# Optimization experiments

Hardware: AMD Instinct MI355X
Metric: run time of the kernel (lower is better)

Reference implementation:

```python
import jax, jax.numpy as jnp
import numpy as np

D_MODEL = 1024
NUM_HEADS = 16
HEAD_DIM = D_MODEL // NUM_HEADS


def setup_inputs() -> dict:
    key = jax.random.key(0)
    kx, kq, kk, kv, ko = jax.random.split(key, 5)
    B, S = 4, 2048
    scale = 1.0 / np.sqrt(D_MODEL)
    return {
        "x": jax.random.normal(kx, (B, S, D_MODEL), dtype=jnp.float32),
        # bias-free linear weights, torch convention [out, in]
        "wq": jax.random.normal(kq, (D_MODEL, D_MODEL), dtype=jnp.float32) * scale,
        "wk": jax.random.normal(kk, (D_MODEL, D_MODEL), dtype=jnp.float32) * scale,
        "wv": jax.random.normal(kv, (D_MODEL, D_MODEL), dtype=jnp.float32) * scale,
        "wo": jax.random.normal(ko, (D_MODEL, D_MODEL), dtype=jnp.float32) * scale,
    }


def reference(x, wq, wk, wv, wo):
    B, S, D = x.shape
    H, Hd = NUM_HEADS, HEAD_DIM
    # projections (y = x @ W^T), reshape to [B, H, S, Hd]
    def proj(w):
        return jnp.einsum('bsd,ed->bse', x, w).reshape(B, S, H, Hd).transpose(0, 2, 1, 3)
    q, k, v = proj(wq), proj(wk), proj(wv)
    # scaled dot-product attention with causal mask
    scores = jnp.einsum('bhqd,bhkd->bhqk', q, k) / jnp.sqrt(jnp.asarray(Hd, x.dtype))
    causal = jnp.tril(jnp.ones((S, S), dtype=bool))  # [S, S]
    scores = jnp.where(causal[None, None], scores, jnp.asarray(-jnp.inf, x.dtype))
    attn = jax.nn.softmax(scores, axis=-1)
    out = jnp.einsum('bhqk,bhkd->bhqd', attn, v)  # [B, H, S, Hd]
    out = out.transpose(0, 2, 1, 3).reshape(B, S, D)
    return jnp.einsum('bsd,ed->bse', out, wo)
```

## Files before the change

### kernel.cpp

```cpp
#include <hip/hip_runtime.h>
#include <hip/hip_bf16.h>
#include <math.h>


#define S_LEN 2048
#define DM    1024
#define NH    16
#define HD    64
#define M_ROWS 8192

typedef __attribute__((ext_vector_type(8))) short bf16x8;
typedef __attribute__((ext_vector_type(4))) float f32x4;

__device__ __forceinline__ float bf2f(unsigned short u) {
  union { unsigned int i; float f; } c; c.i = ((unsigned int)u) << 16; return c.f;
}
__device__ __forceinline__ unsigned short f2bf(float f) {
  unsigned int x = __float_as_uint(f);
  if ((x & 0x7fffffffu) > 0x7f800000u) return (unsigned short)0x7fc0u;
  return (unsigned short)((x + 0x7fffu + ((x >> 16) & 1u)) >> 16);
}
__device__ __forceinline__ unsigned short f2bf_trunc(float f) {
  return (unsigned short)(__float_as_uint(f) >> 16);
}
__device__ __forceinline__ void gl_lds16(const unsigned short* g, unsigned short* l) {
  __builtin_amdgcn_global_load_lds(
      (const __attribute__((address_space(1))) unsigned int*)g,
      (__attribute__((address_space(3))) unsigned int*)l, 16, 0, 0);
}

#define FENCE() asm volatile("" ::: "memory")

__global__ __launch_bounds__(256) void cvt_bf16(const float* __restrict__ in,
                                                unsigned short* __restrict__ out) {
  const int i = blockIdx.x * 256 + threadIdx.x;
  float4 a = ((const float4*)in)[2 * i];
  float4 b = ((const float4*)in)[2 * i + 1];
  ushort4 r0, r1;
  r0.x = f2bf(a.x); r0.y = f2bf(a.y); r0.z = f2bf(a.z); r0.w = f2bf(a.w);
  r1.x = f2bf(b.x); r1.y = f2bf(b.y); r1.z = f2bf(b.z); r1.w = f2bf(b.w);
  ((ushort4*)out)[2 * i] = r0;
  ((ushort4*)out)[2 * i + 1] = r1;
}

__global__ __launch_bounds__(256) void cvt_w3(const float* __restrict__ w0,
                                              const float* __restrict__ w1,
                                              const float* __restrict__ w2,
                                              unsigned short* __restrict__ out) {
  const int idx = blockIdx.x;
  const int which = idx >> 9;
  const float* src = (which == 0) ? w0 : (which == 1) ? w1 : w2;
  unsigned short* dst = out + (size_t)which * (DM * DM);
  const int i = (idx & 511) * 256 + threadIdx.x;
  float4 a = ((const float4*)src)[2 * i];
  float4 b = ((const float4*)src)[2 * i + 1];
  ushort4 r0, r1;
  r0.x = f2bf(a.x); r0.y = f2bf(a.y); r0.z = f2bf(a.z); r0.w = f2bf(a.w);
  r1.x = f2bf(b.x); r1.y = f2bf(b.y); r1.z = f2bf(b.z); r1.w = f2bf(b.w);
  ((ushort4*)dst)[2 * i] = r0;
  ((ushort4*)dst)[2 * i + 1] = r1;
}

template <int OUT_MODE>
__global__ __launch_bounds__(512, 4) void gemm_bt(const unsigned short* __restrict__ A,
                                                  const unsigned short* __restrict__ Wall,
                                                  unsigned short* __restrict__ outB,
                                                  float* __restrict__ outF) {
  __shared__ __align__(16) unsigned short As[3 * 8192];
  __shared__ __align__(16) unsigned short Bs[3 * 4096];
  const int m0 = blockIdx.x * 256;
  const int n0 = blockIdx.y * 128;
  const int tid = threadIdx.x;
  const int lane = tid & 63, w = tid >> 6;
  const int quad = lane >> 4, l15 = lane & 15;
  const int wrow = w >> 1, wcol = w & 1;

  const int skg = w & 3, srq = w >> 2;
  const unsigned short* agA = A    + (size_t)(m0 + srq * 64 + lane) * DM + skg * 8;
  const unsigned short* bgB = Wall + (size_t)(n0 + srq * 64 + lane) * DM + skg * 8;
  const int lA0 = skg * 2048 + srq * 512;
  const int lA1 = lA0 + 1024;
  const int lB  = skg * 1024 + srq * 512;
  const int raA = quad * 2048 + (wrow * 64 + l15) * 8;
  const int raB = quad * 1024 + (wcol * 64 + l15) * 8;

  f32x4 acc[4][4];
#pragma unroll
  for (int i = 0; i < 4; ++i)
#pragma unroll
    for (int j = 0; j < 4; ++j) { acc[i][j].x = 0.f; acc[i][j].y = 0.f; acc[i][j].z = 0.f; acc[i][j].w = 0.f; }

#define STAGE3(T, SB) do {                                                   \
    const unsigned short* ap_ = agA + (size_t)(T) * 32;                      \
    gl_lds16(ap_,          &As[(SB) * 8192 + lA0]);                          \
    gl_lds16(ap_ + 131072, &As[(SB) * 8192 + lA1]);                          \
    gl_lds16(bgB + (size_t)(T) * 32, &Bs[(SB) * 4096 + lB]);                 \
  } while (0)

#define COMPUTE(CB) do {                                                     \
    bf16x8 af_[4], bq_[4];                                                   \
    _Pragma("unroll")                                                        \
    for (int mi = 0; mi < 4; ++mi)                                           \
      af_[mi] = *(const bf16x8*)&As[(CB) * 8192 + raA + mi * 128];           \
    _Pragma("unroll")                                                        \
    for (int ni = 0; ni < 4; ++ni)                                           \
      bq_[ni] = *(const bf16x8*)&Bs[(CB) * 4096 + raB + ni * 128];           \
    __builtin_amdgcn_s_setprio(1);                                           \
    _Pragma("unroll")                                                        \
    for (int mi = 0; mi < 4; ++mi)                                           \
      _Pragma("unroll")                                                      \
      for (int ni = 0; ni < 4; ++ni)                                         \
        acc[mi][ni] = __builtin_amdgcn_mfma_f32_16x16x32_bf16(af_[mi], bq_[ni], acc[mi][ni], 0, 0, 0); \
    __builtin_amdgcn_s_setprio(0);                                           \
  } while (0)

#define SUBSTEP(T, SB, CB) do {                                              \
    FENCE();                                                                 \
    STAGE3((T), (SB));                                                       \
    asm volatile("s_waitcnt vmcnt(6)" ::: "memory");                         \
    __builtin_amdgcn_s_barrier();                                            \
    FENCE();                                                                 \
    COMPUTE(CB);                                                             \
    FENCE();                                                                 \
    __builtin_amdgcn_s_barrier();                                            \
  } while (0)

  STAGE3(0, 0);
  STAGE3(1, 1);

  for (int t = 0; t < 30; t += 3) {
    SUBSTEP(t + 2, 2, 0);
    SUBSTEP(t + 3, 0, 1);
    SUBSTEP(t + 4, 1, 2);
  }
  asm volatile("s_waitcnt vmcnt(3)" ::: "memory");
  __builtin_amdgcn_s_barrier();
  FENCE();
  COMPUTE(0);
  FENCE();
  __builtin_amdgcn_s_barrier();
  asm volatile("s_waitcnt vmcnt(0)" ::: "memory");
  __builtin_amdgcn_s_barrier();
  FENCE();
  COMPUTE(1);

#undef SUBSTEP
#undef COMPUTE
#undef STAGE3

  const float oscale = (OUT_MODE == 0 && n0 < 1024) ? 0.125f : 1.0f;
#pragma unroll
  for (int mi = 0; mi < 4; ++mi) {
#pragma unroll
    for (int reg = 0; reg < 4; ++reg) {
      const int m = m0 + wrow * 64 + mi * 16 + quad * 4 + reg;
#pragma unroll
      for (int ni = 0; ni < 4; ++ni) {
        const int e = n0 + wcol * 64 + ni * 16 + l15;
        const float v = acc[mi][ni][reg];
        if (OUT_MODE == 0) {
          const int z = e >> 10;
          const int e10 = e & 1023;
          const int b = m >> 11, s = m & (S_LEN - 1);
          const int h = e10 >> 6, hd = e10 & 63;
          outB[(size_t)z * (M_ROWS * DM) +
               (((size_t)(b * NH + h)) * S_LEN + s) * HD + hd] = f2bf(v * oscale);
        } else {
          outF[(size_t)m * DM + e] = v;
        }
      }
    }
  }
}

__global__ __launch_bounds__(256) void attn_mfma(const unsigned short* __restrict__ Q,
                                                 const unsigned short* __restrict__ K,
                                                 const unsigned short* __restrict__ V,
                                                 unsigned short* __restrict__ O) {
  __shared__ unsigned short Ks[64][72];
  __shared__ unsigned short Vt[64][72];
  __shared__ unsigned short Pl[4][16][72];
  const int bh  = blockIdx.x;
  const int t   = blockIdx.y;
  const int tid = threadIdx.x;
  const int w    = tid >> 6;
  const int lane = tid & 63;
  const int quad = lane >> 4;
  const int l15  = lane & 15;

  const size_t base = (size_t)bh * S_LEN * HD;
  const int kr0 = tid >> 3, kc0 = (tid & 7) * 8;
  const int vs = (tid & 31) * 2, vh = (tid >> 5) * 8;
  const int b = bh >> 4, h = bh & 15;

  for (int phase = 0; phase < 2; ++phase) {
    const int bx  = phase ? (31 - t) : t;
    const int wq0 = bx * 64 + w * 16;

    bf16x8 qa[2];
#pragma unroll
    for (int st = 0; st < 2; ++st)
      qa[st] = *(const bf16x8*)(Q + base + (size_t)(wq0 + l15) * HD + st * 32 + quad * 8);

    f32x4 o[4];
#pragma unroll
    for (int sub = 0; sub < 4; ++sub) { o[sub].x = 0.f; o[sub].y = 0.f; o[sub].z = 0.f; o[sub].w = 0.f; }
    float l_i[4] = {0.f, 0.f, 0.f, 0.f};

    const int jtmax = bx;
    for (int jt = 0; jt <= jtmax; ++jt) {
      __syncthreads();
      {
        const unsigned short* kb = K + base + (size_t)jt * 64 * HD;
        const unsigned short* vb = V + base + (size_t)jt * 64 * HD;
        *(uint4*)&Ks[kr0][kc0]      = *(const uint4*)(kb + kr0 * HD + kc0);
        *(uint4*)&Ks[kr0 + 32][kc0] = *(const uint4*)(kb + (kr0 + 32) * HD + kc0);
        union { uint4 v; unsigned short u[8]; } r0, r1;
        r0.v = *(const uint4*)(vb + (size_t)vs * HD + vh);
        r1.v = *(const uint4*)(vb + (size_t)(vs + 1) * HD + vh);
#pragma unroll
        for (int j = 0; j < 8; ++j)
          *(unsigned int*)&Vt[vh + j][vs] = (unsigned int)r0.u[j] | ((unsigned int)r1.u[j] << 16);
      }
      __syncthreads();

      const int rel = jt * 64 - wq0;
      const bool partial = (rel >= -63);
      const int submax = partial ? (((15 - rel) >> 4) + 1) : 4;
      const int steps  = partial ? ((submax + 1) >> 1) : 2;

      f32x4 s[4];
#pragma unroll
      for (int sub = 0; sub < 4; ++sub) {
        if (sub < submax) {
          bf16x8 kb0 = *(const bf16x8*)&Ks[sub * 16 + l15][quad * 8];
          bf16x8 kb1 = *(const bf16x8*)&Ks[sub * 16 + l15][quad * 8 + 32];
          f32x4 acc = {0.f, 0.f, 0.f, 0.f};
          acc = __builtin_amdgcn_mfma_f32_16x16x32_bf16(qa[0], kb0, acc, 0, 0, 0);
          acc = __builtin_amdgcn_mfma_f32_16x16x32_bf16(qa[1], kb1, acc, 0, 0, 0);
          s[sub] = acc;
        }
      }

#pragma unroll
      for (int reg = 0; reg < 4; ++reg) {
        float ls = 0.f;
#pragma unroll
        for (int sub = 0; sub < 4; ++sub) {
          if (sub < submax) {
            float v = s[sub][reg];
            if (partial) {
              const int c = jt * 64 + sub * 16 + l15;
              const int r = wq0 + quad * 4 + reg;
              v = (r >= c) ? v : -1.0e30f;
            }
            const float p = __expf(v);
            ls += p;
            Pl[w][quad * 4 + reg][sub * 16 + l15] = f2bf_trunc(p);
          } else {
            Pl[w][quad * 4 + reg][sub * 16 + l15] = 0;
          }
        }
        l_i[reg] += ls;
      }

#pragma unroll
      for (int st = 0; st < 2; ++st) {
        if (st < steps) {
          bf16x8 pa = *(const bf16x8*)&Pl[w][l15][st * 32 + quad * 8];
#pragma unroll
          for (int sub = 0; sub < 4; ++sub) {
            bf16x8 vv = *(const bf16x8*)&Vt[sub * 16 + l15][st * 32 + quad * 8];
            o[sub] = __builtin_amdgcn_mfma_f32_16x16x32_bf16(pa, vv, o[sub], 0, 0, 0);
          }
        }
      }
    }

#pragma unroll
    for (int reg = 0; reg < 4; ++reg) {
      float lt = l_i[reg];
      lt += __shfl_xor(lt, 1);
      lt += __shfl_xor(lt, 2);
      lt += __shfl_xor(lt, 4);
      lt += __shfl_xor(lt, 8);
      const float inv = 1.0f / lt;
      const int sg = wq0 + quad * 4 + reg;
#pragma unroll
      for (int sub = 0; sub < 4; ++sub) {
        O[((size_t)(b * S_LEN + sg)) * DM + h * HD + sub * 16 + l15] = f2bf(o[sub][reg] * inv);
      }
    }
  }
}

extern "C" void kernel_launch(void* const* d_in, const int* in_sizes, int n_in,
                              void* d_out, int out_size, void* d_ws, size_t ws_size,
                              hipStream_t stream) {
  const float* x  = (const float*)d_in[0];
  const float* wq = (const float*)d_in[1];
  const float* wk = (const float*)d_in[2];
  const float* wv = (const float*)d_in[3];
  const float* wo = (const float*)d_in[4];

  unsigned short* Qb = (unsigned short*)d_ws;
  unsigned short* Kb = Qb + (size_t)M_ROWS * DM;
  unsigned short* Vb = Kb + (size_t)M_ROWS * DM;
  unsigned short* Xb = Vb + (size_t)M_ROWS * DM;
  unsigned short* Ob = Xb;
  (void)Kb; (void)Vb;

  unsigned short* Wstash = (unsigned short*)d_out;

  dim3 bb(256);
  dim3 gb(512);

  hipLaunchKernelGGL(cvt_bf16, dim3((M_ROWS * DM) / 2048), bb, 0, stream, x, Xb);
  hipLaunchKernelGGL(cvt_w3, dim3(3 * (DM * DM) / 2048), bb, 0, stream, wq, wk, wv, Wstash);
  hipLaunchKernelGGL((gemm_bt<0>), dim3(M_ROWS / 256, 3 * DM / 128), gb, 0, stream,
                     Xb, Wstash, Qb, (float*)nullptr);
  hipLaunchKernelGGL(attn_mfma, dim3(64, 16), bb, 0, stream, Qb, Qb + (size_t)M_ROWS * DM,
                     Qb + 2 * (size_t)M_ROWS * DM, Ob);
  hipLaunchKernelGGL(cvt_bf16, dim3((DM * DM) / 2048), bb, 0, stream, wo, Qb);
  hipLaunchKernelGGL((gemm_bt<1>), dim3(M_ROWS / 256, DM / 128), gb, 0, stream,
                     Ob, Qb, (unsigned short*)nullptr, (float*)d_out);
}
```

Before: 230.0 us.

## Prefetch next K/V tile into registers and transpose score MFMA for packed P stores

Loads the next K/V tile into registers while the current tile is computed, hiding global load latency behind the MFMA work. Swaps the MFMA operands so each lane holds four consecutive key scores for one query row, which lets P be written to LDS as packed uint2 stores and reduces the row-sum to a single accumulator with fewer shuffles. Uses v_perm to build the V transpose and bf16 packing, and raises wave priority around the MFMA sections. The cost is extra live registers for the prefetch and more complex lane bookkeeping for normalization.

```diff
diff --git a/kernel.cpp b/kernel.cpp
--- a/kernel.cpp
+++ b/kernel.cpp
@@ -19,9 +19,6 @@
   unsigned int x = __float_as_uint(f);
   if ((x & 0x7fffffffu) > 0x7f800000u) return (unsigned short)0x7fc0u;
   return (unsigned short)((x + 0x7fffu + ((x >> 16) & 1u)) >> 16);
-}
-__device__ __forceinline__ unsigned short f2bf_trunc(float f) {
-  return (unsigned short)(__float_as_uint(f) >> 16);
 }
 __device__ __forceinline__ void gl_lds16(const unsigned short* g, unsigned short* l) {
   __builtin_amdgcn_global_load_lds(
@@ -196,6 +193,7 @@
   for (int phase = 0; phase < 2; ++phase) {
     const int bx  = phase ? (31 - t) : t;
     const int wq0 = bx * 64 + w * 16;
+    const int qrow = wq0 + l15;
 
     bf16x8 qa[2];
 #pragma unroll
@@ -205,24 +203,43 @@
     f32x4 o[4];
 #pragma unroll
     for (int sub = 0; sub < 4; ++sub) { o[sub].x = 0.f; o[sub].y = 0.f; o[sub].z = 0.f; o[sub].w = 0.f; }
-    float l_i[4] = {0.f, 0.f, 0.f, 0.f};
+    float l_acc = 0.f;
 
     const int jtmax = bx;
+
+    uint4 krA, krB, vrA, vrB;
+    {
+      const unsigned short* kbp = K + base;
+      const unsigned short* vbp = V + base;
+      krA = *(const uint4*)(kbp + kr0 * HD + kc0);
+      krB = *(const uint4*)(kbp + (kr0 + 32) * HD + kc0);
+      vrA = *(const uint4*)(vbp + (size_t)vs * HD + vh);
+      vrB = *(const uint4*)(vbp + (size_t)(vs + 1) * HD + vh);
+    }
+
     for (int jt = 0; jt <= jtmax; ++jt) {
       __syncthreads();
+      *(uint4*)&Ks[kr0][kc0]      = krA;
+      *(uint4*)&Ks[kr0 + 32][kc0] = krB;
       {
-        const unsigned short* kb = K + base + (size_t)jt * 64 * HD;
-        const unsigned short* vb = V + base + (size_t)jt * 64 * HD;
-        *(uint4*)&Ks[kr0][kc0]      = *(const uint4*)(kb + kr0 * HD + kc0);
-        *(uint4*)&Ks[kr0 + 32][kc0] = *(const uint4*)(kb + (kr0 + 32) * HD + kc0);
-        union { uint4 v; unsigned short u[8]; } r0, r1;
-        r0.v = *(const uint4*)(vb + (size_t)vs * HD + vh);
-        r1.v = *(const uint4*)(vb + (size_t)(vs + 1) * HD + vh);
-#pragma unroll
-        for (int j = 0; j < 8; ++j)
-          *(unsigned int*)&Vt[vh + j][vs] = (unsigned int)r0.u[j] | ((unsigned int)r1.u[j] << 16);
+        const unsigned int* a0 = (const unsigned int*)&vrA;
+        const unsigned int* a1 = (const unsigned int*)&vrB;
+#pragma unroll
+        for (int i = 0; i < 4; ++i) {
+          *(unsigned int*)&Vt[vh + 2 * i][vs]     = __builtin_amdgcn_perm(a1[i], a0[i], 0x05040100u);
+          *(unsigned int*)&Vt[vh + 2 * i + 1][vs] = __builtin_amdgcn_perm(a1[i], a0[i], 0x07060302u);
+        }
       }
       __syncthreads();
+
+      if (jt < jtmax) {
+        const unsigned short* kbp = K + base + (size_t)(jt + 1) * 64 * HD;
+        const unsigned short* vbp = V + base + (size_t)(jt + 1) * 64 * HD;
+        krA = *(const uint4*)(kbp + kr0 * HD + kc0);
+        krB = *(const uint4*)(kbp + (kr0 + 32) * HD + kc0);
+        vrA = *(const uint4*)(vbp + (size_t)vs * HD + vh);
+        vrB = *(const uint4*)(vbp + (size_t)(vs + 1) * HD + vh);
+      }
 
       const int rel = jt * 64 - wq0;
       const bool partial = (rel >= -63);
@@ -230,40 +247,47 @@
       const int steps  = partial ? ((submax + 1) >> 1) : 2;
 
       f32x4 s[4];
+      __builtin_amdgcn_s_setprio(1);
 #pragma unroll
       for (int sub = 0; sub < 4; ++sub) {
         if (sub < submax) {
           bf16x8 kb0 = *(const bf16x8*)&Ks[sub * 16 + l15][quad * 8];
           bf16x8 kb1 = *(const bf16x8*)&Ks[sub * 16 + l15][quad * 8 + 32];
           f32x4 acc = {0.f, 0.f, 0.f, 0.f};
-          acc = __builtin_amdgcn_mfma_f32_16x16x32_bf16(qa[0], kb0, acc, 0, 0, 0);
-          acc = __builtin_amdgcn_mfma_f32_16x16x32_bf16(qa[1], kb1, acc, 0, 0, 0);
+          acc = __builtin_amdgcn_mfma_f32_16x16x32_bf16(kb0, qa[0], acc, 0, 0, 0);
+          acc = __builtin_amdgcn_mfma_f32_16x16x32_bf16(kb1, qa[1], acc, 0, 0, 0);
           s[sub] = acc;
         }
       }
-
-#pragma unroll
-      for (int reg = 0; reg < 4; ++reg) {
-        float ls = 0.f;
-#pragma unroll
-        for (int sub = 0; sub < 4; ++sub) {
-          if (sub < submax) {
-            float v = s[sub][reg];
+      __builtin_amdgcn_s_setprio(0);
+
+#pragma unroll
+      for (int sub = 0; sub < 4; ++sub) {
+        if (sub < submax) {
+          float p0, p1, p2, p3;
+          {
+            float v0 = s[sub][0], v1 = s[sub][1], v2 = s[sub][2], v3 = s[sub][3];
             if (partial) {
-              const int c = jt * 64 + sub * 16 + l15;
-              const int r = wq0 + quad * 4 + reg;
-              v = (r >= c) ? v : -1.0e30f;
+              const int kb = jt * 64 + sub * 16 + quad * 4;
+              v0 = (qrow >= kb)     ? v0 : -1.0e30f;
+              v1 = (qrow >= kb + 1) ? v1 : -1.0e30f;
+              v2 = (qrow >= kb + 2) ? v2 : -1.0e30f;
+              v3 = (qrow >= kb + 3) ? v3 : -1.0e30f;
             }
-            const float p = __expf(v);
-            ls += p;
-            Pl[w][quad * 4 + reg][sub * 16 + l15] = f2bf_trunc(p);
-          } else {
-            Pl[w][quad * 4 + reg][sub * 16 + l15] = 0;
+            p0 = __expf(v0); p1 = __expf(v1); p2 = __expf(v2); p3 = __expf(v3);
           }
-        }
-        l_i[reg] += ls;
-      }
-
+          l_acc += (p0 + p1) + (p2 + p3);
+          uint2 dd;
+          dd.x = __builtin_amdgcn_perm(__float_as_uint(p1), __float_as_uint(p0), 0x07060302u);
+          dd.y = __builtin_amdgcn_perm(__float_as_uint(p3), __float_as_uint(p2), 0x07060302u);
+          *(uint2*)&Pl[w][l15][sub * 16 + quad * 4] = dd;
+        } else {
+          uint2 zz; zz.x = 0u; zz.y = 0u;
+          *(uint2*)&Pl[w][l15][sub * 16 + quad * 4] = zz;
+        }
+      }
+
+      __builtin_amdgcn_s_setprio(1);
 #pragma unroll
       for (int st = 0; st < 2; ++st) {
         if (st < steps) {
@@ -275,20 +299,20 @@
           }
         }
       }
+      __builtin_amdgcn_s_setprio(0);
     }
 
+    float lt = l_acc;
+    lt += __shfl_xor(lt, 16);
+    lt += __shfl_xor(lt, 32);
+    const float inv = 1.0f / lt;
 #pragma unroll
     for (int reg = 0; reg < 4; ++reg) {
-      float lt = l_i[reg];
-      lt += __shfl_xor(lt, 1);
-      lt += __shfl_xor(lt, 2);
-      lt += __shfl_xor(lt, 4);
-      lt += __shfl_xor(lt, 8);
-      const float inv = 1.0f / lt;
+      const float invr = __shfl(inv, quad * 20 + reg);
       const int sg = wq0 + quad * 4 + reg;
 #pragma unroll
       for (int sub = 0; sub < 4; ++sub) {
-        O[((size_t)(b * S_LEN + sg)) * DM + h * HD + sub * 16 + l15] = f2bf(o[sub][reg] * inv);
+        O[((size_t)(b * S_LEN + sg)) * DM + h * HD + sub * 16 + l15] = f2bf(o[sub][reg] * invr);
       }
     }
   }
```

New measurement: 253.9 us. +10.4%, slower.

## Rewrite attention kernel with 32x32 MFMA tiles and register-resident P

Applied to the files above, without the earlier changes.

The attention kernel now uses 32x32x16 bf16 MFMA instructions with 128-query blocks and 32 queries per wave, computing S transposed so the probabilities can be repacked into the PV operand through register permutes and a cross-half shuffle instead of a round trip through shared memory. The paired-phase load balancing is dropped in favour of reversed block ordering over 16 query tiles, and the V transpose uses byte-permute instructions. It also adds s_setprio around the MFMA sections and a launch-bounds occupancy hint. The aim is to cut LDS traffic and instruction count per tile. Larger per-wave accumulators raise register pressure, and without the pairing the causal workload per block is less balanced.

```diff
diff --git a/kernel.cpp b/kernel.cpp
--- a/kernel.cpp
+++ b/kernel.cpp
@@ -11,6 +11,7 @@
 
 typedef __attribute__((ext_vector_type(8))) short bf16x8;
 typedef __attribute__((ext_vector_type(4))) float f32x4;
+typedef __attribute__((ext_vector_type(16))) float f32x16;
 
 __device__ __forceinline__ float bf2f(unsigned short u) {
   union { unsigned int i; float f; } c; c.i = ((unsigned int)u) << 16; return c.f;
@@ -19,9 +20,6 @@
   unsigned int x = __float_as_uint(f);
   if ((x & 0x7fffffffu) > 0x7f800000u) return (unsigned short)0x7fc0u;
   return (unsigned short)((x + 0x7fffu + ((x >> 16) & 1u)) >> 16);
-}
-__device__ __forceinline__ unsigned short f2bf_trunc(float f) {
-  return (unsigned short)(__float_as_uint(f) >> 16);
 }
 __device__ __forceinline__ void gl_lds16(const unsigned short* g, unsigned short* l) {
   __builtin_amdgcn_global_load_lds(
@@ -173,124 +171,124 @@
   }
 }
 
-__global__ __launch_bounds__(256) void attn_mfma(const unsigned short* __restrict__ Q,
-                                                 const unsigned short* __restrict__ K,
-                                                 const unsigned short* __restrict__ V,
-                                                 unsigned short* __restrict__ O) {
+__global__ __launch_bounds__(256, 4) void attn_mfma(const unsigned short* __restrict__ Q,
+                                                    const unsigned short* __restrict__ K,
+                                                    const unsigned short* __restrict__ V,
+                                                    unsigned short* __restrict__ O) {
   __shared__ unsigned short Ks[64][72];
   __shared__ unsigned short Vt[64][72];
-  __shared__ unsigned short Pl[4][16][72];
-  const int bh  = blockIdx.x;
-  const int t   = blockIdx.y;
+  const int bh = blockIdx.x;
+  const int bx = 15 - (int)blockIdx.y;
   const int tid = threadIdx.x;
-  const int w    = tid >> 6;
-  const int lane = tid & 63;
-  const int quad = lane >> 4;
-  const int l15  = lane & 15;
-
+  const int w = tid >> 6, lane = tid & 63;
+  const int l31 = lane & 31, hi = lane >> 5;
   const size_t base = (size_t)bh * S_LEN * HD;
+  const int b = bh >> 4, h = bh & 15;
+  const int wq0 = bx * 128 + w * 32;
+  const int diag_jt = 2 * bx + (w >> 1);
+  const int jt_blk = 2 * bx + 1;
   const int kr0 = tid >> 3, kc0 = (tid & 7) * 8;
   const int vs = (tid & 31) * 2, vh = (tid >> 5) * 8;
-  const int b = bh >> 4, h = bh & 15;
-
-  for (int phase = 0; phase < 2; ++phase) {
-    const int bx  = phase ? (31 - t) : t;
-    const int wq0 = bx * 64 + w * 16;
-
-    bf16x8 qa[2];
-#pragma unroll
-    for (int st = 0; st < 2; ++st)
-      qa[st] = *(const bf16x8*)(Q + base + (size_t)(wq0 + l15) * HD + st * 32 + quad * 8);
-
-    f32x4 o[4];
-#pragma unroll
-    for (int sub = 0; sub < 4; ++sub) { o[sub].x = 0.f; o[sub].y = 0.f; o[sub].z = 0.f; o[sub].w = 0.f; }
-    float l_i[4] = {0.f, 0.f, 0.f, 0.f};
-
-    const int jtmax = bx;
-    for (int jt = 0; jt <= jtmax; ++jt) {
-      __syncthreads();
-      {
-        const unsigned short* kb = K + base + (size_t)jt * 64 * HD;
-        const unsigned short* vb = V + base + (size_t)jt * 64 * HD;
-        *(uint4*)&Ks[kr0][kc0]      = *(const uint4*)(kb + kr0 * HD + kc0);
-        *(uint4*)&Ks[kr0 + 32][kc0] = *(const uint4*)(kb + (kr0 + 32) * HD + kc0);
-        union { uint4 v; unsigned short u[8]; } r0, r1;
-        r0.v = *(const uint4*)(vb + (size_t)vs * HD + vh);
-        r1.v = *(const uint4*)(vb + (size_t)(vs + 1) * HD + vh);
-#pragma unroll
-        for (int j = 0; j < 8; ++j)
-          *(unsigned int*)&Vt[vh + j][vs] = (unsigned int)r0.u[j] | ((unsigned int)r1.u[j] << 16);
-      }
-      __syncthreads();
-
-      const int rel = jt * 64 - wq0;
-      const bool partial = (rel >= -63);
-      const int submax = partial ? (((15 - rel) >> 4) + 1) : 4;
-      const int steps  = partial ? ((submax + 1) >> 1) : 2;
-
-      f32x4 s[4];
-#pragma unroll
-      for (int sub = 0; sub < 4; ++sub) {
-        if (sub < submax) {
-          bf16x8 kb0 = *(const bf16x8*)&Ks[sub * 16 + l15][quad * 8];
-          bf16x8 kb1 = *(const bf16x8*)&Ks[sub * 16 + l15][quad * 8 + 32];
-          f32x4 acc = {0.f, 0.f, 0.f, 0.f};
-          acc = __builtin_amdgcn_mfma_f32_16x16x32_bf16(qa[0], kb0, acc, 0, 0, 0);
-          acc = __builtin_amdgcn_mfma_f32_16x16x32_bf16(qa[1], kb1, acc, 0, 0, 0);
-          s[sub] = acc;
-        }
-      }
-
-#pragma unroll
-      for (int reg = 0; reg < 4; ++reg) {
-        float ls = 0.f;
-#pragma unroll
-        for (int sub = 0; sub < 4; ++sub) {
-          if (sub < submax) {
-            float v = s[sub][reg];
-            if (partial) {
-              const int c = jt * 64 + sub * 16 + l15;
-              const int r = wq0 + quad * 4 + reg;
-              v = (r >= c) ? v : -1.0e30f;
-            }
-            const float p = __expf(v);
-            ls += p;
-            Pl[w][quad * 4 + reg][sub * 16 + l15] = f2bf_trunc(p);
-          } else {
-            Pl[w][quad * 4 + reg][sub * 16 + l15] = 0;
-          }
-        }
-        l_i[reg] += ls;
-      }
-
-#pragma unroll
-      for (int st = 0; st < 2; ++st) {
-        if (st < steps) {
-          bf16x8 pa = *(const bf16x8*)&Pl[w][l15][st * 32 + quad * 8];
-#pragma unroll
-          for (int sub = 0; sub < 4; ++sub) {
-            bf16x8 vv = *(const bf16x8*)&Vt[sub * 16 + l15][st * 32 + quad * 8];
-            o[sub] = __builtin_amdgcn_mfma_f32_16x16x32_bf16(pa, vv, o[sub], 0, 0, 0);
-          }
-        }
+
+  bf16x8 qb[4];
+#pragma unroll
+  for (int ds = 0; ds < 4; ++ds)
+    qb[ds] = *(const bf16x8*)(Q + base + (size_t)(wq0 + l31) * HD + ds * 16 + hi * 8);
+
+  f32x16 o0, o1;
+#pragma unroll
+  for (int r = 0; r < 16; ++r) { o0[r] = 0.f; o1[r] = 0.f; }
+  float l_acc = 0.f;
+
+  for (int jt = 0; jt <= jt_blk; ++jt) {
+    __syncthreads();
+    {
+      const unsigned short* kgp = K + base + (size_t)jt * 64 * HD;
+      const unsigned short* vgp = V + base + (size_t)jt * 64 * HD;
+      *(uint4*)&Ks[kr0][kc0]      = *(const uint4*)(kgp + kr0 * HD + kc0);
+      *(uint4*)&Ks[kr0 + 32][kc0] = *(const uint4*)(kgp + (kr0 + 32) * HD + kc0);
+      uint4 r0 = *(const uint4*)(vgp + (size_t)vs * HD + vh);
+      uint4 r1 = *(const uint4*)(vgp + (size_t)(vs + 1) * HD + vh);
+      const unsigned int* a0 = (const unsigned int*)&r0;
+      const unsigned int* a1 = (const unsigned int*)&r1;
+#pragma unroll
+      for (int j = 0; j < 4; ++j) {
+        *(unsigned int*)&Vt[vh + 2 * j][vs]     = __builtin_amdgcn_perm(a1[j], a0[j], 0x05040100u);
+        *(unsigned int*)&Vt[vh + 2 * j + 1][vs] = __builtin_amdgcn_perm(a1[j], a0[j], 0x07060302u);
       }
     }
-
-#pragma unroll
-    for (int reg = 0; reg < 4; ++reg) {
-      float lt = l_i[reg];
-      lt += __shfl_xor(lt, 1);
-      lt += __shfl_xor(lt, 2);
-      lt += __shfl_xor(lt, 4);
-      lt += __shfl_xor(lt, 8);
-      const float inv = 1.0f / lt;
-      const int sg = wq0 + quad * 4 + reg;
-#pragma unroll
-      for (int sub = 0; sub < 4; ++sub) {
-        O[((size_t)(b * S_LEN + sg)) * DM + h * HD + sub * 16 + l15] = f2bf(o[sub][reg] * inv);
+    __syncthreads();
+
+    if (jt <= diag_jt) {
+      const bool diag = (jt == diag_jt);
+      for (int kb = 0; kb < 2; ++kb) {
+        const bool kb_zero = diag && ((w & 1) == 0) && (kb == 1);
+        const bool kb_part = diag && (kb == (w & 1));
+        if (kb_zero) continue;
+
+        f32x16 sa;
+#pragma unroll
+        for (int r = 0; r < 16; ++r) sa[r] = 0.f;
+        __builtin_amdgcn_s_setprio(1);
+#pragma unroll
+        for (int ds = 0; ds < 4; ++ds) {
+          bf16x8 kf = *(const bf16x8*)&Ks[kb * 32 + l31][ds * 16 + hi * 8];
+          sa = __builtin_amdgcn_mfma_f32_32x32x16_bf16(kf, qb[ds], sa, 0, 0, 0);
+        }
+        __builtin_amdgcn_s_setprio(0);
+
+        float p[16];
+        if (kb_part) {
+#pragma unroll
+          for (int r = 0; r < 16; ++r) {
+            const int krel = (r & 3) + 8 * (r >> 2) + 4 * hi;
+            p[r] = __expf((l31 >= krel) ? sa[r] : -1.0e30f);
+          }
+        } else {
+#pragma unroll
+          for (int r = 0; r < 16; ++r) p[r] = __expf(sa[r]);
+        }
+        l_acc += (((p[0] + p[1]) + (p[2] + p[3])) + ((p[4] + p[5]) + (p[6] + p[7])))
+               + (((p[8] + p[9]) + (p[10] + p[11])) + ((p[12] + p[13]) + (p[14] + p[15])));
+
+        unsigned int pk[8], sk[8];
+#pragma unroll
+        for (int g = 0; g < 4; ++g) {
+          pk[2 * g]     = __builtin_amdgcn_perm(__float_as_uint(p[4 * g + 1]), __float_as_uint(p[4 * g]),     0x07060302u);
+          pk[2 * g + 1] = __builtin_amdgcn_perm(__float_as_uint(p[4 * g + 3]), __float_as_uint(p[4 * g + 2]), 0x07060302u);
+        }
+#pragma unroll
+        for (int i = 0; i < 8; ++i) sk[i] = (unsigned int)__shfl_xor((int)pk[i], 32);
+
+#pragma unroll
+        for (int sl = 0; sl < 2; ++sl) {
+          const int g0 = 2 * sl, g1 = 2 * sl + 1;
+          union { unsigned int u[4]; bf16x8 v; } fa;
+          fa.u[0] = hi ? sk[2 * g1]     : pk[2 * g0];
+          fa.u[1] = hi ? sk[2 * g1 + 1] : pk[2 * g0 + 1];
+          fa.u[2] = hi ? pk[2 * g1]     : sk[2 * g0];
+          fa.u[3] = hi ? pk[2 * g1 + 1] : sk[2 * g0 + 1];
+          const int s = kb * 2 + sl;
+          bf16x8 v0 = *(const bf16x8*)&Vt[l31][s * 16 + hi * 8];
+          bf16x8 v1 = *(const bf16x8*)&Vt[32 + l31][s * 16 + hi * 8];
+          __builtin_amdgcn_s_setprio(1);
+          o0 = __builtin_amdgcn_mfma_f32_32x32x16_bf16(fa.v, v0, o0, 0, 0, 0);
+          o1 = __builtin_amdgcn_mfma_f32_32x32x16_bf16(fa.v, v1, o1, 0, 0, 0);
+          __builtin_amdgcn_s_setprio(0);
+        }
       }
     }
+  }
+
+  const float lf = l_acc + __shfl_xor(l_acc, 32);
+  const float inv = 1.0f / lf;
+#pragma unroll
+  for (int r = 0; r < 16; ++r) {
+    const int qrel = (r & 3) + 8 * (r >> 2) + 4 * hi;
+    const float invr = __shfl(inv, qrel);
+    const size_t orow = (size_t)(b * S_LEN + wq0 + qrel) * DM + h * HD;
+    O[orow + l31]      = f2bf(o0[r] * invr);
+    O[orow + 32 + l31] = f2bf(o1[r] * invr);
   }
 }
 
```

Measured after the change: 199.6 us. -13.2%, faster.
